# Kernel optimization log

Measured on AMD Instinct MI355X. Metric: run time of the kernel, lower is better.

The kernel has to match this reference:

```python
import jax, jax.numpy as jnp
import numpy as np

B, N, CC, CF, H, W = 4, 4, 256, 512, 128, 128
h, w = H // 2, W // 2


def _upsample2x(x):
    return jnp.repeat(jnp.repeat(x, 2, axis=2), 2, axis=3)


def setup_inputs() -> dict:
    key = jax.random.key(0)
    ks = jax.random.split(key, 8)
    return {
        "contexts": jax.random.normal(ks[0], (B, N, CC, H, W), dtype=jnp.float32),
        "mainstream": jax.random.normal(ks[1], (B, CF, h, w), dtype=jnp.float32),
        "Wc_w": jax.random.normal(ks[2], (CC, CC), dtype=jnp.float32) * 0.02,  # 1x1 conv Cc->Cc
        "Wc_b": jnp.zeros((CC,), dtype=jnp.float32),
        "Wf_w": jax.random.normal(ks[3], (CC, CF), dtype=jnp.float32) * 0.02,  # 1x1 conv Cf->Cc
        "Wf_b": jnp.zeros((CC,), dtype=jnp.float32),
        "Wv_w": jax.random.normal(ks[4], (CC, CF, 3, 3), dtype=jnp.float32) * 0.02,  # 3x3 conv Cf->Cc
        "Wv_b": jnp.zeros((CC,), dtype=jnp.float32),
    }


def reference(contexts, mainstream, Wc_w, Wc_b, Wf_w, Wf_b, Wv_w, Wv_b):
    # queries: 1x1 conv Cf->Cc on mainstream  [B,Cc,h,w]
    queries = jnp.einsum('oc,bchw->bohw', Wf_w, mainstream) + Wf_b[None, :, None, None]
    # keys: 1x1 conv Cc->Cc applied to every context  [B,N,Cc,H,W]
    keys = jnp.einsum('oc,bnchw->bnohw', Wc_w, contexts) + Wc_b[None, None, :, None, None]
    # values: 3x3 conv Cf->Cc, padding 1  [B,Cc,h,w]
    values = jax.lax.conv_general_dilated(
        mainstream, Wv_w, window_strides=(1, 1), padding='SAME',
        dimension_numbers=('NCHW', 'OIHW', 'NCHW')) + Wv_b[None, :, None, None]
    q_up = _upsample2x(queries)   # [B,Cc,H,W]
    v_up = _upsample2x(values)    # [B,Cc,H,W]
    # per-pixel attention scores over the N contexts
    scores = jnp.einsum('bnchw,bchw->bnhw', keys, q_up)      # [B,N,H,W]
    attn = jax.nn.softmax(scores, axis=1)                    # softmax over contexts
    attn_out = jnp.einsum('bnchw,bnhw->bchw', contexts, attn)
    return attn_out + v_up
```

## Files before the change

kernel.cpp:

```cpp
#include <hip/hip_runtime.h>

#define NB   4
#define NN   4
#define CCh  256
#define CFh  512
#define HH   128
#define WW   128
#define PLO  4096
#define PHI  16384

typedef __bf16 bf16;
typedef __bf16 bf16x8 __attribute__((ext_vector_type(8)));
typedef float  f32x4  __attribute__((ext_vector_type(4)));
typedef float  f32x2  __attribute__((ext_vector_type(2)));

__device__ __forceinline__ void gll16(const void* g, void* lds) {
    __builtin_amdgcn_global_load_lds(
        (const __attribute__((address_space(1))) void*)g,
        (__attribute__((address_space(3))) void*)lds, 16, 0, 0);
}

__global__ void prep_mqk(const float* __restrict__ Wc_w, const float* __restrict__ Wf_w,
                         const float* __restrict__ Wf_b, bf16* __restrict__ M_qk,
                         float* __restrict__ d_qk) {
    int c = blockIdx.y;
    int f = blockIdx.x * 256 + threadIdx.x;
    float s = 0.f;
    for (int o = 0; o < CCh; ++o)
        s += Wc_w[o * CCh + c] * Wf_w[o * CFh + f];
    M_qk[c * CFh + f] = (bf16)s;
    if (blockIdx.x == 0 && threadIdx.x == 0) {
        float d = 0.f;
        for (int o = 0; o < CCh; ++o) d += Wc_w[o * CCh + c] * Wf_b[o];
        d_qk[c] = d;
    }
}

__global__ void prep_ms(const float* __restrict__ ms, bf16* __restrict__ ms_t) {
    __shared__ float tile[32][33];
    int b = blockIdx.z;
    int p0 = blockIdx.x * 32, f0 = blockIdx.y * 32;
    int tx = threadIdx.x;
    int r = tx >> 5, cc = tx & 31;
    const float* src = ms + (size_t)b * CFh * PLO;
#pragma unroll
    for (int q = 0; q < 4; ++q) {
        int fl = q * 8 + r;
        tile[fl][cc] = src[(size_t)(f0 + fl) * PLO + p0 + cc];
    }
    __syncthreads();
    bf16* dst = ms_t + (size_t)b * PLO * CFh;
#pragma unroll
    for (int q = 0; q < 4; ++q) {
        int pl = q * 8 + r;
        dst[(size_t)(p0 + pl) * CFh + f0 + cc] = (bf16)tile[cc][pl];
    }
}

__global__ void prep_wv(const float* __restrict__ Wv_w, bf16* __restrict__ Wv_p,
                        bf16* __restrict__ zerob) {
    int tid = blockIdx.x * 256 + threadIdx.x;
    int t = tid / (CCh * CFh);
    int rem = tid % (CCh * CFh);
    int c = rem / CFh, f = rem % CFh;
    Wv_p[tid] = (bf16)Wv_w[(size_t)(c * CFh + f) * 9 + t];
    if (tid < 1024) zerob[tid] = (bf16)0.f;
}

__global__ __launch_bounds__(256) void gemm_kernel(
    const bf16* __restrict__ Wv_p,
    const bf16* __restrict__ M_qk,
    const bf16* __restrict__ ms_t,
    const float* __restrict__ d_qk,
    const bf16* __restrict__ zerob,
    float* __restrict__ v3, bf16* __restrict__ qk_out) {
    __shared__ __align__(16) bf16 Alds[128 * 32];
    __shared__ __align__(16) bf16 Blds[128 * 32];

    const int tx = threadIdx.x;
    const int wave = tx >> 6, lane = tx & 63;
    const int ptile = blockIdx.x, ctile = blockIdx.y;
    const int z = blockIdx.z;
    const int mode = (z >= 12);
    const int b = mode ? (z - 12) : (z / 3);
    const int tg = mode ? 0 : (z % 3);
    const int t0 = tg * 3;
    const int ntaps = mode ? 1 : 3;

    const bf16* Wbase = mode ? M_qk : (Wv_p + (size_t)t0 * CCh * CFh);
    const bf16* msb = ms_t + (size_t)b * PLO * CFh;

    int idx0 = wave * 2048 + lane * 16;
    int idx1 = idx0 + 1024;
    int rA0 = idx0 >> 6, fq0 = (idx0 >> 4) & 3;
    int rA1 = idx1 >> 6, fq1 = (idx1 >> 4) & 3;
    const size_t aoff0 = (size_t)(ctile * 128 + rA0) * CFh + fq0 * 8;
    const size_t aoff1 = (size_t)(ctile * 128 + rA1) * CFh + fq1 * 8;
    char* ldsA0 = (char*)Alds + wave * 2048;
    char* ldsA1 = ldsA0 + 1024;
    char* ldsB0 = (char*)Blds + wave * 2048;
    char* ldsB1 = ldsB0 + 1024;

    const int p0 = ptile * 128 + rA0, p1 = ptile * 128 + rA1;
    const int i0 = p0 >> 6, j0 = p0 & 63;
    const int i1 = p1 >> 6, j1 = p1 & 63;

    f32x4 acc[4][4];
#pragma unroll
    for (int mi = 0; mi < 4; ++mi)
#pragma unroll
        for (int ni = 0; ni < 4; ++ni) acc[mi][ni] = f32x4{0.f, 0.f, 0.f, 0.f};

    const int wm = wave >> 1, wn = wave & 1;
    const int quad = lane >> 4, l15 = lane & 15;

    for (int t = 0; t < ntaps; ++t) {
        const int dy = mode ? 0 : ((t0 + t) / 3 - 1);
        const int dx = mode ? 0 : ((t0 + t) % 3 - 1);
        const bf16* Wt = Wbase + (size_t)t * CCh * CFh;
        int si0 = i0 + dy, sj0 = j0 + dx, si1 = i1 + dy, sj1 = j1 + dx;
        bool ok0 = (unsigned)si0 < 64u && (unsigned)sj0 < 64u;
        bool ok1 = (unsigned)si1 < 64u && (unsigned)sj1 < 64u;
        const bf16* bsrc0 = ok0 ? msb + (size_t)(si0 * 64 + sj0) * CFh + fq0 * 8 : zerob;
        const bf16* bsrc1 = ok1 ? msb + (size_t)(si1 * 64 + sj1) * CFh + fq1 * 8 : zerob;

        for (int fc = 0; fc < CFh / 32; ++fc) {
            const int f0 = fc * 32;
            __syncthreads();
            gll16(Wt + aoff0 + f0, ldsA0);
            gll16(Wt + aoff1 + f0, ldsA1);
            gll16(bsrc0 + f0, ldsB0);
            gll16(bsrc1 + f0, ldsB1);
            __syncthreads();

            bf16x8 af[4], bfr[4];
#pragma unroll
            for (int mi = 0; mi < 4; ++mi)
                af[mi] = *(const bf16x8*)&Alds[(wm * 64 + mi * 16 + l15) * 32 + quad * 8];
#pragma unroll
            for (int ni = 0; ni < 4; ++ni)
                bfr[ni] = *(const bf16x8*)&Blds[(wn * 64 + ni * 16 + l15) * 32 + quad * 8];
#pragma unroll
            for (int mi = 0; mi < 4; ++mi)
#pragma unroll
                for (int ni = 0; ni < 4; ++ni)
                    acc[mi][ni] = __builtin_amdgcn_mfma_f32_16x16x32_bf16(
                        af[mi], bfr[ni], acc[mi][ni], 0, 0, 0);
        }
    }

    if (mode) {
        bf16* obase = qk_out + (size_t)b * CCh * PLO;
#pragma unroll
        for (int mi = 0; mi < 4; ++mi) {
            int cb = ctile * 128 + wm * 64 + mi * 16 + quad * 4;
#pragma unroll
            for (int ni = 0; ni < 4; ++ni) {
                int p = ptile * 128 + wn * 64 + ni * 16 + l15;
                bf16* op = obase + (size_t)cb * PLO + p;
#pragma unroll
                for (int r = 0; r < 4; ++r)
                    op[(size_t)r * PLO] = (bf16)(acc[mi][ni][r] + d_qk[cb + r]);
            }
        }
    } else {
        float* obase = v3 + (size_t)(tg * NB + b) * CCh * PLO;
#pragma unroll
        for (int mi = 0; mi < 4; ++mi) {
            int cb = ctile * 128 + wm * 64 + mi * 16 + quad * 4;
#pragma unroll
            for (int ni = 0; ni < 4; ++ni) {
                int p = ptile * 128 + wn * 64 + ni * 16 + l15;
                float* op = obase + (size_t)cb * PLO + p;
#pragma unroll
                for (int r = 0; r < 4; ++r)
                    op[(size_t)r * PLO] = acc[mi][ni][r];
            }
        }
    }
}

__global__ __launch_bounds__(512) void attn_kernel(
    const float* __restrict__ ctx,
    const bf16* __restrict__ qk,
    const float* __restrict__ v3,
    const float* __restrict__ Wv_b,
    float* __restrict__ out) {
    __shared__ f32x4 swred[4][8][16];
    const int tx = threadIdx.x;
    const int pq = tx & 15;
    const int cc = tx >> 4;
    const int lane = tx & 63;
    const int wv = tx >> 6;
    const int quad = lane >> 4;

    const int pbase = blockIdx.x << 6;
    const int b = pbase >> 14;
    const int rem = pbase & 16383;
    const int hh = rem >> 7;
    const int w0 = rem & 127;
    const int wq = w0 + pq * 4;
    const int i = hh >> 1, j0 = wq >> 1;

    const int c0 = cc * 8;
    const size_t NSTR = (size_t)CCh * PHI;
    const float* cbase = ctx + (size_t)b * NN * NSTR + (size_t)c0 * PHI
                             + (size_t)hh * WW + wq;
    const bf16* qkb = qk + ((size_t)b * CCh + c0) * PLO + i * 64 + j0;
    const float* vbp = v3 + ((size_t)b * CCh + c0) * PLO + i * 64 + j0;

    f32x4 vals[4][8];
    f32x4 s[4];
#pragma unroll
    for (int n = 0; n < 4; ++n) s[n] = f32x4{0.f, 0.f, 0.f, 0.f};

#pragma unroll
    for (int cj = 0; cj < 8; ++cj) {
        unsigned qw = *(const unsigned*)(qkb + (size_t)cj * PLO);
        float qa = __uint_as_float(qw << 16);
        float qb = __uint_as_float(qw & 0xffff0000u);
        f32x4 qv = {qa, qa, qb, qb};
#pragma unroll
        for (int n = 0; n < 4; ++n) {
            vals[n][cj] = *(const f32x4*)(cbase + n * NSTR + (size_t)cj * PHI);
            s[n] += vals[n][cj] * qv;
        }
    }
#pragma unroll
    for (int n = 0; n < 4; ++n) {
#pragma unroll
        for (int m = 16; m <= 32; m <<= 1) {
            f32x4 t;
            t[0] = __shfl_xor(s[n][0], m);
            t[1] = __shfl_xor(s[n][1], m);
            t[2] = __shfl_xor(s[n][2], m);
            t[3] = __shfl_xor(s[n][3], m);
            s[n] += t;
        }
    }
    f32x4 sq = (quad == 0) ? s[0] : (quad == 1) ? s[1] : (quad == 2) ? s[2] : s[3];
    swred[quad][wv][pq] = sq;
    __syncthreads();

    f32x4 t4[4];
#pragma unroll
    for (int n = 0; n < 4; ++n) {
        f32x4 a = swred[n][0][pq];
#pragma unroll
        for (int w = 1; w < 8; ++w) a += swred[n][w][pq];
        t4[n] = a;
    }
    f32x4 mx;
#pragma unroll
    for (int k = 0; k < 4; ++k)
        mx[k] = fmaxf(fmaxf(t4[0][k], t4[1][k]), fmaxf(t4[2][k], t4[3][k]));
    f32x4 e[4];
#pragma unroll
    for (int n = 0; n < 4; ++n)
#pragma unroll
        for (int k = 0; k < 4; ++k) e[n][k] = __expf(t4[n][k] - mx[k]);
    f32x4 ssum = e[0] + e[1] + e[2] + e[3];
    f32x4 a4[4];
#pragma unroll
    for (int n = 0; n < 4; ++n)
#pragma unroll
        for (int k = 0; k < 4; ++k) a4[n][k] = e[n][k] / ssum[k];

    float* outp = out + ((size_t)b * CCh + c0) * PHI + (size_t)hh * WW + wq;
#pragma unroll
    for (int cj = 0; cj < 8; ++cj) {
        f32x2 vv = *(const f32x2*)(vbp + (size_t)cj * PLO);
        vv += *(const f32x2*)(vbp + 4194304 + (size_t)cj * PLO);
        vv += *(const f32x2*)(vbp + 8388608 + (size_t)cj * PLO);
        float bc = Wv_b[c0 + cj];
        float va = vv[0] + bc, vb2 = vv[1] + bc;
        f32x4 o = vals[0][cj] * a4[0] + vals[1][cj] * a4[1] +
                  vals[2][cj] * a4[2] + vals[3][cj] * a4[3] +
                  f32x4{va, va, vb2, vb2};
        *(f32x4*)(outp + (size_t)cj * PHI) = o;
    }
}

extern "C" void kernel_launch(void* const* d_in, const int* in_sizes, int n_in,
                              void* d_out, int out_size, void* d_ws, size_t ws_size,
                              hipStream_t stream) {
    const float* ctx  = (const float*)d_in[0];
    const float* ms   = (const float*)d_in[1];
    const float* Wc_w = (const float*)d_in[2];
    const float* Wf_w = (const float*)d_in[4];
    const float* Wf_b = (const float*)d_in[5];
    const float* Wv_w = (const float*)d_in[6];
    const float* Wv_b = (const float*)d_in[7];
    float* out = (float*)d_out;

    char* ws = (char*)d_ws;
    bf16*  ms_t  = (bf16*)ws;
    bf16*  Wv_p  = (bf16*)(ws + 16777216);
    bf16*  M_qk  = (bf16*)(ws + 19136512);
    float* d_qk  = (float*)(ws + 19398656);
    bf16*  zerob = (bf16*)(ws + 19399680);
    bf16*  qk    = (bf16*)(ws + 19401728);
    float* v3    = (float*)(ws + 27790336);

    prep_mqk<<<dim3(2, 256), 256, 0, stream>>>(Wc_w, Wf_w, Wf_b, M_qk, d_qk);
    prep_ms<<<dim3(128, 16, 4), 256, 0, stream>>>(ms, ms_t);
    prep_wv<<<dim3(4608), 256, 0, stream>>>(Wv_w, Wv_p, zerob);
    gemm_kernel<<<dim3(32, 2, 16), 256, 0, stream>>>(Wv_p, M_qk, ms_t, d_qk,
                                                     zerob, v3, qk);
    attn_kernel<<<dim3(1024), 512, 0, stream>>>(ctx, qk, v3, Wv_b, out);
}
```

Before: 513.2 us.

## Fuse prep kernels, store value partials in bf16, reshape attention blocks

Merges the three preprocessing kernels into a single launch that dispatches on block index, removing two launch overheads. The 3x3-conv partial sums are now written and read as bf16 rather than fp32, halving that intermediate traffic at some cost in precision. The attention kernel is reorganised into 256-thread blocks covering 16 pixels with 4 channels per thread, using a wider shuffle reduction and a smaller LDS reduction, so more blocks run with fewer registers each.

```diff
diff --git a/kernel.cpp b/kernel.cpp
--- a/kernel.cpp
+++ b/kernel.cpp
@@ -12,7 +12,6 @@
 typedef __bf16 bf16;
 typedef __bf16 bf16x8 __attribute__((ext_vector_type(8)));
 typedef float  f32x4  __attribute__((ext_vector_type(4)));
-typedef float  f32x2  __attribute__((ext_vector_type(2)));
 
 __device__ __forceinline__ void gll16(const void* g, void* lds) {
     __builtin_amdgcn_global_load_lds(
@@ -20,51 +19,55 @@
         (__attribute__((address_space(3))) void*)lds, 16, 0, 0);
 }
 
-__global__ void prep_mqk(const float* __restrict__ Wc_w, const float* __restrict__ Wf_w,
-                         const float* __restrict__ Wf_b, bf16* __restrict__ M_qk,
-                         float* __restrict__ d_qk) {
-    int c = blockIdx.y;
-    int f = blockIdx.x * 256 + threadIdx.x;
-    float s = 0.f;
-    for (int o = 0; o < CCh; ++o)
-        s += Wc_w[o * CCh + c] * Wf_w[o * CFh + f];
-    M_qk[c * CFh + f] = (bf16)s;
-    if (blockIdx.x == 0 && threadIdx.x == 0) {
-        float d = 0.f;
-        for (int o = 0; o < CCh; ++o) d += Wc_w[o * CCh + c] * Wf_b[o];
-        d_qk[c] = d;
-    }
-}
-
-__global__ void prep_ms(const float* __restrict__ ms, bf16* __restrict__ ms_t) {
+__device__ __forceinline__ float bflo(unsigned u) { return __uint_as_float(u << 16); }
+__device__ __forceinline__ float bfhi(unsigned u) { return __uint_as_float(u & 0xffff0000u); }
+
+__global__ __launch_bounds__(256) void prep_all(
+    const float* __restrict__ Wc_w, const float* __restrict__ Wf_w,
+    const float* __restrict__ Wf_b, const float* __restrict__ ms,
+    const float* __restrict__ Wv_w,
+    bf16* __restrict__ M_qk, float* __restrict__ d_qk,
+    bf16* __restrict__ ms_t, bf16* __restrict__ Wv_p, bf16* __restrict__ zerob) {
     __shared__ float tile[32][33];
-    int b = blockIdx.z;
-    int p0 = blockIdx.x * 32, f0 = blockIdx.y * 32;
-    int tx = threadIdx.x;
-    int r = tx >> 5, cc = tx & 31;
-    const float* src = ms + (size_t)b * CFh * PLO;
-#pragma unroll
-    for (int q = 0; q < 4; ++q) {
-        int fl = q * 8 + r;
-        tile[fl][cc] = src[(size_t)(f0 + fl) * PLO + p0 + cc];
-    }
-    __syncthreads();
-    bf16* dst = ms_t + (size_t)b * PLO * CFh;
-#pragma unroll
-    for (int q = 0; q < 4; ++q) {
-        int pl = q * 8 + r;
-        dst[(size_t)(p0 + pl) * CFh + f0 + cc] = (bf16)tile[cc][pl];
-    }
-}
-
-__global__ void prep_wv(const float* __restrict__ Wv_w, bf16* __restrict__ Wv_p,
-                        bf16* __restrict__ zerob) {
-    int tid = blockIdx.x * 256 + threadIdx.x;
-    int t = tid / (CCh * CFh);
-    int rem = tid % (CCh * CFh);
-    int c = rem / CFh, f = rem % CFh;
-    Wv_p[tid] = (bf16)Wv_w[(size_t)(c * CFh + f) * 9 + t];
-    if (tid < 1024) zerob[tid] = (bf16)0.f;
+    const int bid = blockIdx.x, tx = threadIdx.x;
+    if (bid < 512) {
+        int c = bid >> 1;
+        int f = (bid & 1) * 256 + tx;
+        float s = 0.f;
+#pragma unroll 8
+        for (int o = 0; o < CCh; ++o)
+            s += Wc_w[o * CCh + c] * Wf_w[o * CFh + f];
+        M_qk[c * CFh + f] = (bf16)s;
+        if ((bid & 1) == 0 && tx == 0) {
+            float d = 0.f;
+            for (int o = 0; o < CCh; ++o) d += Wc_w[o * CCh + c] * Wf_b[o];
+            d_qk[c] = d;
+        }
+    } else if (bid < 8704) {
+        int id = bid - 512;
+        int b = id >> 11, f0 = ((id >> 7) & 15) * 32, p0 = (id & 127) * 32;
+        int r = tx >> 5, cc = tx & 31;
+        const float* src = ms + (size_t)b * CFh * PLO;
+#pragma unroll
+        for (int q = 0; q < 4; ++q) {
+            int fl = q * 8 + r;
+            tile[fl][cc] = src[(size_t)(f0 + fl) * PLO + p0 + cc];
+        }
+        __syncthreads();
+        bf16* dst = ms_t + (size_t)b * PLO * CFh;
+#pragma unroll
+        for (int q = 0; q < 4; ++q) {
+            int pl = q * 8 + r;
+            dst[(size_t)(p0 + pl) * CFh + f0 + cc] = (bf16)tile[cc][pl];
+        }
+    } else {
+        int tid = (bid - 8704) * 256 + tx;
+        int t = tid / (CCh * CFh);
+        int rem = tid % (CCh * CFh);
+        int c = rem / CFh, f = rem % CFh;
+        Wv_p[tid] = (bf16)Wv_w[(size_t)(c * CFh + f) * 9 + t];
+        if (tid < 1024) zerob[tid] = (bf16)0.f;
+    }
 }
 
 __global__ __launch_bounds__(256) void gemm_kernel(
@@ -73,7 +76,7 @@
     const bf16* __restrict__ ms_t,
     const float* __restrict__ d_qk,
     const bf16* __restrict__ zerob,
-    float* __restrict__ v3, bf16* __restrict__ qk_out) {
+    bf16* __restrict__ vpart, bf16* __restrict__ qk_out) {
     __shared__ __align__(16) bf16 Alds[128 * 32];
     __shared__ __align__(16) bf16 Blds[128 * 32];
 
@@ -164,37 +167,36 @@
             }
         }
     } else {
-        float* obase = v3 + (size_t)(tg * NB + b) * CCh * PLO;
+        bf16* obase = vpart + (size_t)(tg * NB + b) * CCh * PLO;
 #pragma unroll
         for (int mi = 0; mi < 4; ++mi) {
             int cb = ctile * 128 + wm * 64 + mi * 16 + quad * 4;
 #pragma unroll
             for (int ni = 0; ni < 4; ++ni) {
                 int p = ptile * 128 + wn * 64 + ni * 16 + l15;
-                float* op = obase + (size_t)cb * PLO + p;
+                bf16* op = obase + (size_t)cb * PLO + p;
 #pragma unroll
                 for (int r = 0; r < 4; ++r)
-                    op[(size_t)r * PLO] = acc[mi][ni][r];
+                    op[(size_t)r * PLO] = (bf16)acc[mi][ni][r];
             }
         }
     }
 }
 
-__global__ __launch_bounds__(512) void attn_kernel(
+__global__ __launch_bounds__(256, 3) void attn_kernel(
     const float* __restrict__ ctx,
     const bf16* __restrict__ qk,
-    const float* __restrict__ v3,
+    const bf16* __restrict__ vpart,
     const float* __restrict__ Wv_b,
     float* __restrict__ out) {
-    __shared__ f32x4 swred[4][8][16];
+    __shared__ f32x4 swred[4][4][4];
     const int tx = threadIdx.x;
-    const int pq = tx & 15;
-    const int cc = tx >> 4;
-    const int lane = tx & 63;
-    const int wv = tx >> 6;
-    const int quad = lane >> 4;
-
-    const int pbase = blockIdx.x << 6;
+    const int pq = tx & 3;
+    const int cz = tx >> 2;
+    const int lane = tx & 63, wv = tx >> 6;
+    const int c0 = cz * 4;
+
+    const int pbase = blockIdx.x << 4;
     const int b = pbase >> 14;
     const int rem = pbase & 16383;
     const int hh = rem >> 7;
@@ -202,23 +204,20 @@
     const int wq = w0 + pq * 4;
     const int i = hh >> 1, j0 = wq >> 1;
 
-    const int c0 = cc * 8;
     const size_t NSTR = (size_t)CCh * PHI;
-    const float* cbase = ctx + (size_t)b * NN * NSTR + (size_t)c0 * PHI
-                             + (size_t)hh * WW + wq;
+    const float* cbase = ctx + ((size_t)b * NN * CCh + c0) * PHI + (size_t)hh * WW + wq;
     const bf16* qkb = qk + ((size_t)b * CCh + c0) * PLO + i * 64 + j0;
-    const float* vbp = v3 + ((size_t)b * CCh + c0) * PLO + i * 64 + j0;
-
-    f32x4 vals[4][8];
+    const bf16* vb  = vpart + ((size_t)b * CCh + c0) * PLO + i * 64 + j0;
+
+    f32x4 vals[4][4];
     f32x4 s[4];
 #pragma unroll
     for (int n = 0; n < 4; ++n) s[n] = f32x4{0.f, 0.f, 0.f, 0.f};
 
 #pragma unroll
-    for (int cj = 0; cj < 8; ++cj) {
+    for (int cj = 0; cj < 4; ++cj) {
         unsigned qw = *(const unsigned*)(qkb + (size_t)cj * PLO);
-        float qa = __uint_as_float(qw << 16);
-        float qb = __uint_as_float(qw & 0xffff0000u);
+        float qa = bflo(qw), qb = bfhi(qw);
         f32x4 qv = {qa, qa, qb, qb};
 #pragma unroll
         for (int n = 0; n < 4; ++n) {
@@ -229,7 +228,7 @@
 #pragma unroll
     for (int n = 0; n < 4; ++n) {
 #pragma unroll
-        for (int m = 16; m <= 32; m <<= 1) {
+        for (int m = 4; m <= 32; m <<= 1) {
             f32x4 t;
             t[0] = __shfl_xor(s[n][0], m);
             t[1] = __shfl_xor(s[n][1], m);
@@ -238,18 +237,15 @@
             s[n] += t;
         }
     }
-    f32x4 sq = (quad == 0) ? s[0] : (quad == 1) ? s[1] : (quad == 2) ? s[2] : s[3];
-    swred[quad][wv][pq] = sq;
+    int npub = (lane >> 2) & 3;
+    f32x4 sq = (npub == 0) ? s[0] : (npub == 1) ? s[1] : (npub == 2) ? s[2] : s[3];
+    if (lane < 16) swred[wv][lane & 3][npub] = sq;
     __syncthreads();
 
     f32x4 t4[4];
 #pragma unroll
-    for (int n = 0; n < 4; ++n) {
-        f32x4 a = swred[n][0][pq];
-#pragma unroll
-        for (int w = 1; w < 8; ++w) a += swred[n][w][pq];
-        t4[n] = a;
-    }
+    for (int n = 0; n < 4; ++n)
+        t4[n] = swred[0][pq][n] + swred[1][pq][n] + swred[2][pq][n] + swred[3][pq][n];
     f32x4 mx;
 #pragma unroll
     for (int k = 0; k < 4; ++k)
@@ -266,17 +262,19 @@
 #pragma unroll
         for (int k = 0; k < 4; ++k) a4[n][k] = e[n][k] / ssum[k];
 
+    const size_t TGS = (size_t)NB * CCh * PLO;
+    f32x4 bcv = *(const f32x4*)(Wv_b + c0);
     float* outp = out + ((size_t)b * CCh + c0) * PHI + (size_t)hh * WW + wq;
 #pragma unroll
-    for (int cj = 0; cj < 8; ++cj) {
-        f32x2 vv = *(const f32x2*)(vbp + (size_t)cj * PLO);
-        vv += *(const f32x2*)(vbp + 4194304 + (size_t)cj * PLO);
-        vv += *(const f32x2*)(vbp + 8388608 + (size_t)cj * PLO);
-        float bc = Wv_b[c0 + cj];
-        float va = vv[0] + bc, vb2 = vv[1] + bc;
+    for (int cj = 0; cj < 4; ++cj) {
+        unsigned u0 = *(const unsigned*)(vb + (size_t)cj * PLO);
+        unsigned u1 = *(const unsigned*)(vb + TGS + (size_t)cj * PLO);
+        unsigned u2 = *(const unsigned*)(vb + 2 * TGS + (size_t)cj * PLO);
+        float va  = bflo(u0) + bflo(u1) + bflo(u2) + bcv[cj];
+        float vbb = bfhi(u0) + bfhi(u1) + bfhi(u2) + bcv[cj];
         f32x4 o = vals[0][cj] * a4[0] + vals[1][cj] * a4[1] +
                   vals[2][cj] * a4[2] + vals[3][cj] * a4[3] +
-                  f32x4{va, va, vb2, vb2};
+                  f32x4{va, va, vbb, vbb};
         *(f32x4*)(outp + (size_t)cj * PHI) = o;
     }
 }
@@ -300,12 +298,11 @@
     float* d_qk  = (float*)(ws + 19398656);
     bf16*  zerob = (bf16*)(ws + 19399680);
     bf16*  qk    = (bf16*)(ws + 19401728);
-    float* v3    = (float*)(ws + 27790336);
-
-    prep_mqk<<<dim3(2, 256), 256, 0, stream>>>(Wc_w, Wf_w, Wf_b, M_qk, d_qk);
-    prep_ms<<<dim3(128, 16, 4), 256, 0, stream>>>(ms, ms_t);
-    prep_wv<<<dim3(4608), 256, 0, stream>>>(Wv_w, Wv_p, zerob);
+    bf16*  vpart = (bf16*)(ws + 27790336);
+
+    prep_all<<<dim3(13312), 256, 0, stream>>>(Wc_w, Wf_w, Wf_b, ms, Wv_w,
+                                              M_qk, d_qk, ms_t, Wv_p, zerob);
     gemm_kernel<<<dim3(32, 2, 16), 256, 0, stream>>>(Wv_p, M_qk, ms_t, d_qk,
-                                                     zerob, v3, qk);
-    attn_kernel<<<dim3(1024), 512, 0, stream>>>(ctx, qk, v3, Wv_b, out);
-}
+                                                     zerob, vpart, qk);
+    attn_kernel<<<dim3(4096), 256, 0, stream>>>(ctx, qk, vpart, Wv_b, out);
+}
```

After: 544.2 us. 1.06x slower.
